# Optimization experiments

Measured on AMD Instinct MI355X. Metric: run time of the kernel, lower is better.

The kernel has to match this reference:

```python
import jax, jax.numpy as jnp
import numpy as np
from jax import lax

K = 100  # self.k in the module


def setup_inputs() -> dict:
    key = jax.random.key(0)
    k1, k2 = jax.random.split(key)
    query_batch = jax.random.normal(k1, (4, 64, 128), dtype=jnp.float32)  # [B,T,Z]
    targets = jax.random.normal(k2, (100000, 128), dtype=jnp.float32)     # [M,Z]
    return {"query_batch": query_batch, "targets": targets}


def _knn_emissions(query_batch, targets):
    # Brute-force L2 kNN (faiss.IndexFlatL2.search equivalent).
    # sqdist[b,t,m] = ||q_bt - target_m||^2
    qn = jnp.sum(query_batch * query_batch, -1)          # [B,T]
    tn = jnp.sum(targets * targets, -1)                  # [M]
    dots = jnp.einsum('btz,mz->btm', query_batch, targets)
    sqdist = qn[..., None] + tn[None, None, :] - 2.0 * dots  # [B,T,M]
    neg_d, idx = lax.top_k(-sqdist, K)                   # k smallest distances
    distances = -neg_d                                   # [B,T,K]
    # probabilities = exp(-d) / sum exp(-d)  == softmax(-d)
    emit_p = jax.nn.softmax(-distances, axis=-1)         # [B,T,K]
    states = targets[idx]                                # [B,T,K,Z]
    return emit_p, states


def _transition_probs(states):
    # Banded transitions: only between the K states of step t and step t+1.
    # transition_probability(a, b) = exp(-||a-b||^2)  (Gaussian L2 kernel)
    a = states[:, :-1]                                   # [B,T-1,K,Z]
    b = states[:, 1:]                                    # [B,T-1,K,Z]
    d = jnp.sum(a * a, -1)[..., :, None] + jnp.sum(b * b, -1)[..., None, :] \
        - 2.0 * jnp.einsum('btiz,btjz->btij', a, b)      # [B,T-1,K,K]
    return jnp.exp(-d)


def _viterbi_single(emit_p, trans_p):
    # emit_p [T,K], trans_p [T-1,K,K] -> best path indices [T] (int32)
    v0 = emit_p[0]

    def step(v, inp):
        tr, em = inp                                     # [K,K], [K]
        scores = v[:, None] * tr                         # [K,K]
        best = scores.max(axis=0)
        back = jnp.argmax(scores, axis=0)                # [K]
        v_new = best * em
        # rescale to avoid underflow over long T; argmax path unchanged
        v_new = v_new / jnp.maximum(v_new.max(), jnp.float32(1e-30))
        return v_new, back

    v_last, backptrs = lax.scan(step, v0, (trans_p, emit_p[1:]))
    last = jnp.argmax(v_last).astype(jnp.int32)

    def back_step(idx, bp):
        prev = bp[idx].astype(jnp.int32)
        return prev, prev

    _, path_head = lax.scan(back_step, last, backptrs, reverse=True)  # [T-1]
    return jnp.concatenate([path_head, last[None]])      # [T]


def reference(query_batch, targets):
    emit_p, states = _knn_emissions(query_batch, targets)
    trans_p = _transition_probs(states)
    paths = jax.vmap(_viterbi_single)(emit_p, trans_p)   # [B,T]
    # gather selected reference states: [B,T,Z]
    out = jnp.take_along_axis(states, paths[..., None, None], axis=2)[:, :, 0, :]
    return out
```

## Files before the change

kernel.cpp:

```cpp
#include <hip/hip_runtime.h>
#include <cfloat>
#include <climits>
#include <cstdint>
#include <cstddef>

#define ZD    128
#define NQ    256
#define NB    4
#define NT    64
#define KK    100
#define CAP   2048
#define NSAMP 4096
#define RANK  24
#define EPS   3.0f
#define SLABS 256
#define BKT   24
#define TROWS 64
#define QROWS 128
#define LPAD  136

typedef __attribute__((ext_vector_type(8))) short  short8;
typedef __attribute__((ext_vector_type(4))) float  floatx4;
typedef unsigned long long u64;

__device__ inline unsigned short f2bf(float f) {
  unsigned u = __builtin_bit_cast(unsigned, f);
  unsigned r = u + 0x7fffu + ((u >> 16) & 1u);
  return (unsigned short)(r >> 16);
}
__device__ inline unsigned fkey(float f) {
  unsigned u = __builtin_bit_cast(unsigned, f);
  unsigned m = (u & 0x80000000u) ? 0xFFFFFFFFu : 0x80000000u;
  return u ^ m;
}
__device__ inline float unfkey(unsigned k) {
  unsigned u = (k & 0x80000000u) ? (k ^ 0x80000000u) : ~k;
  return __builtin_bit_cast(float, u);
}

__global__ __launch_bounds__(256) void k0_norms(
    const float* __restrict__ Q, const float* __restrict__ T, int M,
    float* __restrict__ qn, float* __restrict__ tn) {
  int gid = blockIdx.x * 256 + threadIdx.x;
  if (gid < M) {
    const float* r = T + (size_t)gid * ZD;
    float s = 0.f;
    #pragma unroll
    for (int z4 = 0; z4 < 32; ++z4) {
      float4 v = *(const float4*)&r[z4 * 4];
      s = fmaf(v.x, v.x, s); s = fmaf(v.y, v.y, s);
      s = fmaf(v.z, v.z, s); s = fmaf(v.w, v.w, s);
    }
    tn[gid] = s;
  } else if (gid < M + NQ) {
    int q = gid - M;
    const float* r = Q + (size_t)q * ZD;
    float s = 0.f;
    #pragma unroll
    for (int z4 = 0; z4 < 32; ++z4) {
      float4 v = *(const float4*)&r[z4 * 4];
      s = fmaf(v.x, v.x, s); s = fmaf(v.y, v.y, s);
      s = fmaf(v.z, v.z, s); s = fmaf(v.w, v.w, s);
    }
    qn[q] = s;
  }
}

__global__ __launch_bounds__(256) void k1a_mfma(
    const float* __restrict__ Q, const float* __restrict__ T,
    const float* __restrict__ qn, const float* __restrict__ tn,
    float* __restrict__ sd_g) {
  __shared__ short Ts[TROWS * LPAD];
  __shared__ short Qs[QROWS * LPAD];
  const int tid = threadIdx.x;
  const int m0 = blockIdx.x * TROWS;
  const int qbase = blockIdx.y * QROWS;

  #pragma unroll
  for (int it = 0; it < 16; ++it) {
    int li = tid + it * 256;
    int row = li >> 5, z4 = li & 31;
    float4 v = *(const float4*)&Q[(size_t)(qbase + row) * ZD + z4 * 4];
    unsigned lo = (unsigned)f2bf(v.x) | ((unsigned)f2bf(v.y) << 16);
    unsigned hi = (unsigned)f2bf(v.z) | ((unsigned)f2bf(v.w) << 16);
    *(uint2*)&Qs[row * LPAD + z4 * 4] = make_uint2(lo, hi);
  }
  #pragma unroll
  for (int it = 0; it < 8; ++it) {
    int li = tid + it * 256;
    int row = li >> 5, z4 = li & 31;
    float4 v = *(const float4*)&T[(size_t)(m0 + row) * ZD + z4 * 4];
    unsigned lo = (unsigned)f2bf(v.x) | ((unsigned)f2bf(v.y) << 16);
    unsigned hi = (unsigned)f2bf(v.z) | ((unsigned)f2bf(v.w) << 16);
    *(uint2*)&Ts[row * LPAD + z4 * 4] = make_uint2(lo, hi);
  }
  __syncthreads();

  const int wave = tid >> 6;
  const int lane = tid & 63;
  const int quad = lane >> 4;
  const int n16  = lane & 15;

  floatx4 acc[8];
  #pragma unroll
  for (int qt = 0; qt < 8; ++qt) acc[qt] = (floatx4)0.f;
  #pragma unroll
  for (int ks = 0; ks < 4; ++ks) {
    short8 a = *(const short8*)&Ts[(wave * 16 + n16) * LPAD + ks * 32 + quad * 8];
    #pragma unroll
    for (int qt = 0; qt < 8; ++qt) {
      short8 b = *(const short8*)&Qs[(qt * 16 + n16) * LPAD + ks * 32 + quad * 8];
      acc[qt] = __builtin_amdgcn_mfma_f32_16x16x32_bf16(a, b, acc[qt], 0, 0, 0);
    }
  }

  const int mbase = m0 + wave * 16 + quad * 4;
  const float4 tnv = *(const float4*)&tn[mbase];
  #pragma unroll
  for (int qt = 0; qt < 8; ++qt) {
    const int q = qbase + qt * 16 + n16;
    const float base = qn[q];
    float4 dv;
    dv.x = fmaf(-2.0f, acc[qt][0], base + tnv.x);
    dv.y = fmaf(-2.0f, acc[qt][1], base + tnv.y);
    dv.z = fmaf(-2.0f, acc[qt][2], base + tnv.z);
    dv.w = fmaf(-2.0f, acc[qt][3], base + tnv.w);
    *(float4*)&sd_g[(size_t)q * NSAMP + mbase] = dv;
  }
}

__global__ __launch_bounds__(256) void k1b_pick(
    const float* __restrict__ sd_g, float* __restrict__ thr) {
  __shared__ float red[256];
  __shared__ int   hist[256];
  const int q = blockIdx.x, tid = threadIdx.x;
  const float* sd = sd_g + (size_t)q * NSAMP;
  float vals[16];
  float lm = FLT_MAX;
  #pragma unroll
  for (int k = 0; k < 16; ++k) {
    vals[k] = sd[k * 256 + tid];
    lm = fminf(lm, vals[k]);
  }
  red[tid] = lm;
  hist[tid] = 0;
  __syncthreads();
  for (int o = 128; o > 0; o >>= 1) {
    if (tid < o) red[tid] = fminf(red[tid], red[tid + o]);
    __syncthreads();
  }
  const float dmin = red[0];
  __syncthreads();
  #pragma unroll
  for (int k = 0; k < 16; ++k) {
    int b = (int)((vals[k] - dmin) * 3.2f);
    b = b < 0 ? 0 : (b > 255 ? 255 : b);
    atomicAdd(&hist[b], 1);
  }
  __syncthreads();
  if (tid == 0) {
    int cum = 0; float Tq = dmin + 80.0f;
    for (int b = 0; b < 256; ++b) {
      cum += hist[b];
      if (cum >= RANK) { Tq = dmin + (float)(b + 1) * 0.3125f; break; }
    }
    thr[q] = Tq;
  }
}

__global__ __launch_bounds__(256, 4) void k2_mfma(
    const float* __restrict__ Q, const float* __restrict__ T, int M, int slabn,
    const float* __restrict__ qn, const float* __restrict__ tn,
    const float* __restrict__ thr,
    int* __restrict__ cnt2, int* __restrict__ sure2, int* __restrict__ cand) {
  __shared__ short Ts[TROWS * LPAD];
  __shared__ short Qs[QROWS * LPAD];
  __shared__ int   lcnt[QROWS];
  __shared__ int   lsure[QROWS];
  __shared__ int   lent[QROWS * BKT];
  const int tid = threadIdx.x;
  const int slab = blockIdx.x;
  const int qbase = blockIdx.y * QROWS;
  const int sbeg = slab * slabn;
  const int send = min(sbeg + slabn, M);

  #pragma unroll
  for (int it = 0; it < 16; ++it) {
    int li = tid + it * 256;
    int row = li >> 5, z4 = li & 31;
    float4 v = *(const float4*)&Q[(size_t)(qbase + row) * ZD + z4 * 4];
    unsigned lo = (unsigned)f2bf(v.x) | ((unsigned)f2bf(v.y) << 16);
    unsigned hi = (unsigned)f2bf(v.z) | ((unsigned)f2bf(v.w) << 16);
    *(uint2*)&Qs[row * LPAD + z4 * 4] = make_uint2(lo, hi);
  }
  if (tid < QROWS) { lcnt[tid] = 0; lsure[tid] = 0; }

  const int wave = tid >> 6;
  const int lane = tid & 63;
  const int quad = lane >> 4;
  const int n16  = lane & 15;

  float baseq[8], tqp[8], tqm[8];
  #pragma unroll
  for (int qt = 0; qt < 8; ++qt) {
    const int q = qbase + qt * 16 + n16;
    float b = qn[q], Tq = thr[q];
    baseq[qt] = b; tqp[qt] = Tq + EPS; tqm[qt] = Tq - EPS;
  }

  float4 pf[8];
  #pragma unroll
  for (int it = 0; it < 8; ++it) {
    int li = tid + it * 256;
    int row = li >> 5, z4 = li & 31;
    int m = sbeg + row;
    pf[it] = make_float4(0.f, 0.f, 0.f, 0.f);
    if (m < send) pf[it] = *(const float4*)&T[(size_t)m * ZD + z4 * 4];
  }

  for (int m0 = sbeg; m0 < send; m0 += TROWS) {
    __syncthreads();
    #pragma unroll
    for (int it = 0; it < 8; ++it) {
      int li = tid + it * 256;
      int row = li >> 5, z4 = li & 31;
      unsigned lo = (unsigned)f2bf(pf[it].x) | ((unsigned)f2bf(pf[it].y) << 16);
      unsigned hi = (unsigned)f2bf(pf[it].z) | ((unsigned)f2bf(pf[it].w) << 16);
      *(uint2*)&Ts[row * LPAD + z4 * 4] = make_uint2(lo, hi);
    }
    __syncthreads();
    if (m0 + TROWS < send) {
      #pragma unroll
      for (int it = 0; it < 8; ++it) {
        int li = tid + it * 256;
        int row = li >> 5, z4 = li & 31;
        int m = m0 + TROWS + row;
        pf[it] = make_float4(0.f, 0.f, 0.f, 0.f);
        if (m < send) pf[it] = *(const float4*)&T[(size_t)m * ZD + z4 * 4];
      }
    }

    floatx4 acc[8];
    #pragma unroll
    for (int qt = 0; qt < 8; ++qt) acc[qt] = (floatx4)0.f;
    #pragma unroll
    for (int ks = 0; ks < 4; ++ks) {
      short8 a = *(const short8*)&Ts[(wave * 16 + n16) * LPAD + ks * 32 + quad * 8];
      #pragma unroll
      for (int qt = 0; qt < 8; ++qt) {
        short8 b = *(const short8*)&Qs[(qt * 16 + n16) * LPAD + ks * 32 + quad * 8];
        acc[qt] = __builtin_amdgcn_mfma_f32_16x16x32_bf16(a, b, acc[qt], 0, 0, 0);
      }
    }

    const int mbase = m0 + wave * 16 + quad * 4;
    float4 tnv = make_float4(0.f, 0.f, 0.f, 0.f);
    if (mbase + 3 < M) tnv = *(const float4*)&tn[mbase];
    else {
      if (mbase + 0 < M) tnv.x = tn[mbase + 0];
      if (mbase + 1 < M) tnv.y = tn[mbase + 1];
      if (mbase + 2 < M) tnv.z = tn[mbase + 2];
    }
    const float tns[4] = {tnv.x, tnv.y, tnv.z, tnv.w};
    #pragma unroll
    for (int qt = 0; qt < 8; ++qt) {
      const int ql = qt * 16 + n16;
      #pragma unroll
      for (int r = 0; r < 4; ++r) {
        const int m = mbase + r;
        float dap = fmaf(-2.0f, acc[qt][r], baseq[qt] + tns[r]);
        if (m < send && dap < tqp[qt]) {
          int pos = atomicAdd(&lcnt[ql], 1);
          if (pos < BKT) lent[ql * BKT + pos] = m;
          if (dap < tqm[qt]) atomicAdd(&lsure[ql], 1);
        }
      }
    }
  }
  __syncthreads();
  if (tid < QROWS) {
    cnt2 [(size_t)(qbase + tid) * SLABS + slab] = lcnt[tid];
    sure2[(size_t)(qbase + tid) * SLABS + slab] = lsure[tid];
  }
  for (int li = tid; li < QROWS * BKT; li += 256) {
    int ql = li / BKT, j = li % BKT;
    int c = lcnt[ql]; if (c > BKT) c = BKT;
    if (j < c)
      cand[((size_t)(qbase + ql) * SLABS + slab) * BKT + j] = lent[li];
  }
}

__global__ __launch_bounds__(256) void k3a_scan(
    const int* __restrict__ cnt2, const int* __restrict__ sure2,
    int* __restrict__ scanx, int* __restrict__ totals, int* __restrict__ validf) {
  const int q = blockIdx.x, tid = threadIdx.x;
  __shared__ int sscan[256];
  __shared__ int ssure, sovf;
  int c = cnt2[(size_t)q * SLABS + tid];
  int su = sure2[(size_t)q * SLABS + tid];
  if (tid == 0) { ssure = 0; sovf = 0; }
  __syncthreads();
  atomicAdd(&ssure, su);
  if (c > BKT) atomicOr(&sovf, 1);
  int val = c;
  sscan[tid] = val;
  __syncthreads();
  for (int o = 1; o < 256; o <<= 1) {
    int add = (tid >= o) ? sscan[tid - o] : 0;
    __syncthreads();
    val += add;
    sscan[tid] = val;
    __syncthreads();
  }
  scanx[(size_t)q * SLABS + tid] = val - c;
  const int total = sscan[255];
  if (tid == 0) {
    totals[q] = total;
    validf[q] = (sovf == 0 && ssure >= KK && total <= CAP) ? 1 : 0;
  }
}

__global__ __launch_bounds__(256) void k3b_rescore(
    const float* __restrict__ Q, const float* __restrict__ T,
    const float* __restrict__ qn, const float* __restrict__ tn,
    const int* __restrict__ cnt2, const int* __restrict__ cand,
    const int* __restrict__ scanx, const int* __restrict__ validf,
    u64* __restrict__ keys) {
  const int q = blockIdx.x, ch = blockIdx.y, tid = threadIdx.x;
  if (!validf[q]) return;
  __shared__ float qv[ZD];
  for (int z = tid; z < ZD; z += 256) qv[z] = Q[(size_t)q * ZD + z];
  __syncthreads();
  const float qnv = qn[q];
  const int slab = ch * 64 + (tid >> 2);
  const int lane = tid & 3;
  const int c = min(cnt2[(size_t)q * SLABS + slab], BKT);
  const int off = scanx[(size_t)q * SLABS + slab];
  for (int k = lane; k < c; k += 4) {
    int idx = cand[((size_t)q * SLABS + slab) * BKT + k];
    const float* r = T + (size_t)idx * ZD;
    float dot = 0.f;
    #pragma unroll 4
    for (int z4 = 0; z4 < 32; ++z4) {
      float4 v = *(const float4*)&r[z4 * 4];
      dot = fmaf(qv[z4 * 4 + 0], v.x, dot);
      dot = fmaf(qv[z4 * 4 + 1], v.y, dot);
      dot = fmaf(qv[z4 * 4 + 2], v.z, dot);
      dot = fmaf(qv[z4 * 4 + 3], v.w, dot);
    }
    float d = fmaf(-2.0f, dot, qnv + tn[idx]);
    keys[(size_t)q * CAP + off + k] = ((u64)fkey(d) << 32) | (unsigned)idx;
  }
}

__global__ __launch_bounds__(256) void k3c_select(
    const float* __restrict__ Q, const float* __restrict__ T, int M,
    const float* __restrict__ qn, const float* __restrict__ tn,
    const int* __restrict__ totals, const int* __restrict__ validf,
    const u64* __restrict__ keys_g,
    int* __restrict__ topi, float* __restrict__ emit) {
  __shared__ u64 key[CAP];
  __shared__ u64 buf[256];
  __shared__ unsigned redA[256], redB[256];
  __shared__ int hist[256];
  __shared__ int hscan[256];
  __shared__ float qv[ZD];
  __shared__ float cd[256];
  __shared__ float sdF[KK];
  __shared__ int   siF[KK];
  __shared__ float ebuf[KK];
  __shared__ float ssum;
  __shared__ int Bb, C2, ccnt, srcFlag;
  __shared__ unsigned kminS; __shared__ int shiftS;
  const int q = blockIdx.x, tid = threadIdx.x;
  const int total = totals[q];
  const bool valid = validf[q] != 0;

  if (valid) {
    for (int i = tid; i < CAP; i += 256)
      key[i] = (i < total) ? keys_g[(size_t)q * CAP + i] : ~0ULL;
    unsigned lmin = 0xFFFFFFFFu, lmax = 0u;
    for (int i = tid; i < total; i += 256) {
      unsigned h = (unsigned)(key[i] >> 32);
      lmin = min(lmin, h); lmax = max(lmax, h);
    }
    redA[tid] = lmin; redB[tid] = lmax;
    hist[tid] = 0;
    __syncthreads();
    for (int o = 128; o > 0; o >>= 1) {
      if (tid < o) {
        redA[tid] = min(redA[tid], redA[tid + o]);
        redB[tid] = max(redB[tid], redB[tid + o]);
      }
      __syncthreads();
    }
    if (tid == 0) {
      unsigned range = redB[0] - redA[0];
      int s = 0;
      while ((range >> s) > 255u) ++s;
      kminS = redA[0]; shiftS = s;
      ccnt = 0;
    }
    __syncthreads();
    const unsigned kmin = kminS; const int sh = shiftS;
    for (int i = tid; i < total; i += 256) {
      int b = (int)(((unsigned)(key[i] >> 32) - kmin) >> sh);
      atomicAdd(&hist[b], 1);
    }
    __syncthreads();
    int v0 = hist[tid];
    hscan[tid] = v0;
    __syncthreads();
    for (int o = 1; o < 256; o <<= 1) {
      int add = (tid >= o) ? hscan[tid - o] : 0;
      __syncthreads();
      v0 += add;
      hscan[tid] = v0;
      __syncthreads();
    }
    if (hscan[tid] >= KK && (tid == 0 || hscan[tid - 1] < KK)) {
      Bb = tid; C2 = hscan[tid];
    }
    __syncthreads();
    const int B = Bb, c2 = C2;
    if (c2 <= 256) {
      for (int i = tid; i < total; i += 256) {
        int b = (int)(((unsigned)(key[i] >> 32) - kmin) >> sh);
        if (b <= B) { int pos = atomicAdd(&ccnt, 1); buf[pos] = key[i]; }
      }
      __syncthreads();
      if (tid >= c2) buf[tid] = ~0ULL;
      __syncthreads();
      for (int k = 2; k <= 256; k <<= 1) {
        for (int j = k >> 1; j > 0; j >>= 1) {
          int x = tid ^ j;
          if (x > tid) {
            u64 a = buf[tid], b2 = buf[x];
            bool asc = ((tid & k) == 0);
            if ((a > b2) == asc) { buf[tid] = b2; buf[x] = a; }
          }
          __syncthreads();
        }
      }
      if (tid == 0) srcFlag = 0;
    } else {
      for (int k = 2; k <= CAP; k <<= 1) {
        for (int j = k >> 1; j > 0; j >>= 1) {
          for (int t = tid; t < CAP; t += 256) {
            int x = t ^ j;
            if (x > t) {
              u64 a = key[t], b2 = key[x];
              bool asc = ((t & k) == 0);
              if ((a > b2) == asc) { key[t] = b2; key[x] = a; }
            }
          }
          __syncthreads();
        }
      }
      if (tid == 0) srcFlag = 1;
    }
    __syncthreads();
  } else {
    for (int z = tid; z < ZD; z += 256) qv[z] = Q[(size_t)q * ZD + z];
    if (tid == 0) {
      for (int k = 0; k < KK; ++k) { sdF[k] = FLT_MAX; siF[k] = INT_MAX; }
      srcFlag = 0;
    }
    __syncthreads();
    const float qnv = qn[q];
    for (int base = 0; base < M; base += 256) {
      int m = base + tid; float d = FLT_MAX;
      if (m < M) {
        const float* r = T + (size_t)m * ZD;
        float dot = 0.f;
        for (int z = 0; z < ZD; ++z) dot = fmaf(qv[z], r[z], dot);
        d = fmaf(-2.0f, dot, qnv + tn[m]);
      }
      cd[tid] = d;
      __syncthreads();
      if (tid == 0) {
        for (int e = 0; e < 256; ++e) {
          float dd = cd[e]; int mm = base + e;
          if (dd < sdF[KK - 1] || (dd == sdF[KK - 1] && mm < siF[KK - 1])) {
            int pos = KK - 1;
            while (pos > 0 && (sdF[pos - 1] > dd || (sdF[pos - 1] == dd && siF[pos - 1] > mm))) {
              sdF[pos] = sdF[pos - 1]; siF[pos] = siF[pos - 1]; --pos;
            }
            sdF[pos] = dd; siF[pos] = mm;
          }
        }
      }
      __syncthreads();
    }
    if (tid < KK) buf[tid] = ((u64)fkey(sdF[tid]) << 32) | (unsigned)siF[tid];
    __syncthreads();
  }

  const int sf = srcFlag;
  if (tid == 0) {
    u64 k0v = sf ? key[0] : buf[0];
    float d0 = unfkey((unsigned)(k0v >> 32));
    float sum = 0.f;
    for (int k = 0; k < KK; ++k) {
      u64 kk = sf ? key[k] : buf[k];
      float e = expf(d0 - unfkey((unsigned)(kk >> 32)));
      ebuf[k] = e; sum += e;
    }
    ssum = sum;
  }
  __syncthreads();
  if (tid < KK) {
    u64 kk = sf ? key[tid] : buf[tid];
    emit[(size_t)q * KK + tid] = ebuf[tid] / ssum;
    topi[(size_t)q * KK + tid] = (int)(kk & 0xFFFFFFFFu);
  }
}

__global__ __launch_bounds__(256) void k4_trans(
    const float* __restrict__ T, const int* __restrict__ topi,
    float* __restrict__ trans) {
  const int bt = blockIdx.x;
  const int b = bt / (NT - 1), t = bt % (NT - 1);
  const int* iA = topi + (size_t)(b * NT + t) * KK;
  const int* iB = topi + (size_t)(b * NT + t + 1) * KK;
  __shared__ float As[KK * 132];
  __shared__ float Bs[KK * 132];
  __shared__ float an[KK];
  __shared__ float bn[KK];
  const int tid = threadIdx.x;
  for (int li = tid; li < KK * 32; li += 256) {
    int row = li >> 5, z4 = li & 31;
    *(float4*)&As[row * 132 + z4 * 4] = *(const float4*)&T[(size_t)iA[row] * ZD + z4 * 4];
    *(float4*)&Bs[row * 132 + z4 * 4] = *(const float4*)&T[(size_t)iB[row] * ZD + z4 * 4];
  }
  __syncthreads();
  if (tid < KK) {
    float s = 0.f;
    for (int z = 0; z < ZD; ++z) s = fmaf(As[tid * 132 + z], As[tid * 132 + z], s);
    an[tid] = s;
  } else if (tid < 2 * KK) {
    int r = tid - KK;
    float s = 0.f;
    for (int z = 0; z < ZD; ++z) s = fmaf(Bs[r * 132 + z], Bs[r * 132 + z], s);
    bn[r] = s;
  }
  __syncthreads();
  const int tx = tid & 15, ty = tid >> 4;
  float acc[7][7];
  #pragma unroll
  for (int k = 0; k < 7; ++k)
    #pragma unroll
    for (int m = 0; m < 7; ++m) acc[k][m] = 0.f;
  int rr[7], cc[7];
  #pragma unroll
  for (int k = 0; k < 7; ++k) { rr[k] = min(ty + 16 * k, KK - 1); cc[k] = min(tx + 16 * k, KK - 1); }
  for (int z4 = 0; z4 < 32; ++z4) {
    float4 a[7], bb[7];
    #pragma unroll
    for (int k = 0; k < 7; ++k) a[k] = *(const float4*)&As[rr[k] * 132 + z4 * 4];
    #pragma unroll
    for (int m = 0; m < 7; ++m) bb[m] = *(const float4*)&Bs[cc[m] * 132 + z4 * 4];
    #pragma unroll
    for (int k = 0; k < 7; ++k)
      #pragma unroll
      for (int m = 0; m < 7; ++m) {
        acc[k][m] = fmaf(a[k].x, bb[m].x, acc[k][m]);
        acc[k][m] = fmaf(a[k].y, bb[m].y, acc[k][m]);
        acc[k][m] = fmaf(a[k].z, bb[m].z, acc[k][m]);
        acc[k][m] = fmaf(a[k].w, bb[m].w, acc[k][m]);
      }
  }
  float* trow = trans + (size_t)bt * KK * KK;
  #pragma unroll
  for (int k = 0; k < 7; ++k) {
    int r = ty + 16 * k;
    if (r < KK) {
      #pragma unroll
      for (int m = 0; m < 7; ++m) {
        int c = tx + 16 * m;
        if (c < KK) {
          float d = fmaf(-2.0f, acc[k][m], an[r] + bn[c]);
          trow[r * KK + c] = expf(-d);
        }
      }
    }
  }
}

__global__ __launch_bounds__(256) void k5_viterbi(
    const float* __restrict__ T, const int* __restrict__ topi,
    const float* __restrict__ emit, const float* __restrict__ trans,
    float* __restrict__ out) {
  const int b = blockIdx.x, tid = threadIdx.x;
  __shared__ float trS[KK * KK];
  __shared__ float v[KK], vn[KK];
  __shared__ float pb[200];
  __shared__ int   pi[200];
  __shared__ int   bpS[(NT - 1) * KK];
  __shared__ int   path[NT];
  __shared__ float maxsh;
  __shared__ int   zflag;

  float4 r[10];
  {
    const float* tr0 = trans + (size_t)(b * (NT - 1)) * KK * KK;
    #pragma unroll
    for (int i = 0; i < 10; ++i) {
      int li = tid + i * 256;
      if (li < 2500) r[i] = *(const float4*)&tr0[li * 4];
    }
  }
  if (tid < KK) v[tid] = emit[(size_t)(b * NT) * KK + tid];
  if (tid == 0) zflag = 0;
  __syncthreads();

  for (int t = 1; t < NT; ++t) {
    #pragma unroll
    for (int i = 0; i < 10; ++i) {
      int li = tid + i * 256;
      if (li < 2500) *(float4*)&trS[li * 4] = r[i];
    }
    __syncthreads();
    if (t < NT - 1) {
      const float* trn = trans + (size_t)(b * (NT - 1) + t) * KK * KK;
      #pragma unroll
      for (int i = 0; i < 10; ++i) {
        int li = tid + i * 256;
        if (li < 2500) r[i] = *(const float4*)&trn[li * 4];
      }
    }
    if (tid < 200) {
      const int j = tid % 100, half = tid / 100;
      const int ia = half * 50, ibnd = ia + 50;
      float best = -FLT_MAX; int bi = ia;
      for (int i = ia; i < ibnd; ++i) {
        float s = v[i] * trS[i * KK + j];
        if (s > best) { best = s; bi = i; }
      }
      pb[tid] = best; pi[tid] = bi;
    }
    __syncthreads();
    if (tid < KK) {
      float b0 = pb[tid], b1 = pb[100 + tid];
      int   i0 = pi[tid], i1 = pi[100 + tid];
      float best = b0; int bi = i0;
      if (b1 > b0) { best = b1; bi = i1; }
      vn[tid] = best * emit[(size_t)(b * NT + t) * KK + tid];
      bpS[(t - 1) * KK + tid] = bi;
    }
    __syncthreads();
    if (tid == 0) {
      float m = vn[0];
      for (int j = 1; j < KK; ++j) m = fmaxf(m, vn[j]);
      maxsh = m;
      if (m == 0.0f) zflag = 1;
    }
    __syncthreads();
    if (tid < KK) v[tid] = vn[tid] / fmaxf(maxsh, 1e-30f);
    __syncthreads();
    if (zflag) {
      for (int li = tid; li < (NT - 1 - t) * KK; li += 256)
        bpS[t * KK + li] = 0;
      __syncthreads();
      break;
    }
  }
  if (tid == 0) {
    float best = -FLT_MAX; int last = 0;
    for (int j = 0; j < KK; ++j) if (v[j] > best) { best = v[j]; last = j; }
    path[NT - 1] = last;
    for (int tt = NT - 2; tt >= 0; --tt)
      path[tt] = bpS[tt * KK + path[tt + 1]];
  }
  __syncthreads();
  for (int li = tid; li < NT * ZD; li += 256) {
    int t = li >> 7, z = li & 127;
    out[(size_t)(b * NT + t) * ZD + z] =
        T[(size_t)topi[(size_t)(b * NT + t) * KK + path[t]] * ZD + z];
  }
}

extern "C" void kernel_launch(void* const* d_in, const int* in_sizes, int n_in,
                              void* d_out, int out_size, void* d_ws, size_t ws_size,
                              hipStream_t stream) {
  const float* Q = (const float*)d_in[0];
  const float* T = (const float*)d_in[1];
  float* out = (float*)d_out;
  const int M = in_sizes[1] / ZD;
  const int slabn = (M + SLABS - 1) / SLABS;

  char* p = (char*)d_ws;
  auto alloc = [&](size_t bytes) -> char* {
    char* r = p; p += (bytes + 511) & ~(size_t)511; return r;
  };
  float* qn     = (float*)alloc((size_t)NQ * 4);
  float* tn     = (float*)alloc((size_t)M * 4);
  float* thr    = (float*)alloc((size_t)NQ * 4);
  float* sd_g   = (float*)alloc((size_t)NQ * NSAMP * 4);
  int*   cnt2   = (int*)  alloc((size_t)NQ * SLABS * 4);
  int*   sure2  = (int*)  alloc((size_t)NQ * SLABS * 4);
  int*   cand   = (int*)  alloc((size_t)NQ * SLABS * BKT * 4);
  int*   scanx  = (int*)  alloc((size_t)NQ * SLABS * 4);
  int*   totals = (int*)  alloc((size_t)NQ * 4);
  int*   validf = (int*)  alloc((size_t)NQ * 4);
  u64*   keys   = (u64*)  alloc((size_t)NQ * CAP * 8);
  int*   topi   = (int*)  alloc((size_t)NQ * KK * 4);
  float* emit   = (float*)alloc((size_t)NQ * KK * 4);
  float* trans  = (float*)alloc((size_t)NB * (NT - 1) * KK * KK * 4);

  const int g0 = (M + NQ + 255) / 256;
  k0_norms<<<g0, 256, 0, stream>>>(Q, T, M, qn, tn);
  dim3 g1a(NSAMP / TROWS, NQ / QROWS);
  k1a_mfma<<<g1a, 256, 0, stream>>>(Q, T, qn, tn, sd_g);
  k1b_pick<<<NQ, 256, 0, stream>>>(sd_g, thr);
  dim3 g2(SLABS, NQ / QROWS);
  k2_mfma<<<g2, 256, 0, stream>>>(Q, T, M, slabn, qn, tn, thr, cnt2, sure2, cand);
  k3a_scan<<<NQ, 256, 0, stream>>>(cnt2, sure2, scanx, totals, validf);
  dim3 g3b(NQ, 4);
  k3b_rescore<<<g3b, 256, 0, stream>>>(Q, T, qn, tn, cnt2, cand, scanx, validf, keys);
  k3c_select<<<NQ, 256, 0, stream>>>(Q, T, M, qn, tn, totals, validf, keys, topi, emit);
  k4_trans<<<NB * (NT - 1), 256, 0, stream>>>(T, topi, trans);
  k5_viterbi<<<NB, 256, 0, stream>>>(T, topi, emit, trans, out);
}
```

Measured before the change: 250.8 us.

## Halve query tile in k2 and drop register prefetch of target rows

The k2 filtering kernel now processes 64 queries per block instead of 128, doubling the grid to 1024 blocks and halving per-block accumulators, LDS, and atomics. The software register prefetch of the next target tile is removed, so target loads now happen directly before the LDS store in each iteration. This is meant to improve parallelism and cut register pressure. In exchange, each target tile is read from memory twice as often and there is no longer any overlap of global loads with MFMA work.

```diff
diff --git a/kernel.cpp b/kernel.cpp
--- a/kernel.cpp
+++ b/kernel.cpp
@@ -17,6 +17,7 @@
 #define BKT   24
 #define TROWS 64
 #define QROWS 128
+#define QR2   64
 #define LPAD  136
 
 typedef __attribute__((ext_vector_type(8))) short  short8;
@@ -168,24 +169,24 @@
   }
 }
 
-__global__ __launch_bounds__(256, 4) void k2_mfma(
+__global__ __launch_bounds__(256, 3) void k2_mfma(
     const float* __restrict__ Q, const float* __restrict__ T, int M, int slabn,
     const float* __restrict__ qn, const float* __restrict__ tn,
     const float* __restrict__ thr,
     int* __restrict__ cnt2, int* __restrict__ sure2, int* __restrict__ cand) {
   __shared__ short Ts[TROWS * LPAD];
-  __shared__ short Qs[QROWS * LPAD];
-  __shared__ int   lcnt[QROWS];
-  __shared__ int   lsure[QROWS];
-  __shared__ int   lent[QROWS * BKT];
+  __shared__ short Qs[QR2 * LPAD];
+  __shared__ int   lcnt[QR2];
+  __shared__ int   lsure[QR2];
+  __shared__ int   lent[QR2 * BKT];
   const int tid = threadIdx.x;
   const int slab = blockIdx.x;
-  const int qbase = blockIdx.y * QROWS;
+  const int qbase = blockIdx.y * QR2;
   const int sbeg = slab * slabn;
   const int send = min(sbeg + slabn, M);
 
   #pragma unroll
-  for (int it = 0; it < 16; ++it) {
+  for (int it = 0; it < 8; ++it) {
     int li = tid + it * 256;
     int row = li >> 5, z4 = li & 31;
     float4 v = *(const float4*)&Q[(size_t)(qbase + row) * ZD + z4 * 4];
@@ -193,61 +194,44 @@
     unsigned hi = (unsigned)f2bf(v.z) | ((unsigned)f2bf(v.w) << 16);
     *(uint2*)&Qs[row * LPAD + z4 * 4] = make_uint2(lo, hi);
   }
-  if (tid < QROWS) { lcnt[tid] = 0; lsure[tid] = 0; }
+  if (tid < QR2) { lcnt[tid] = 0; lsure[tid] = 0; }
 
   const int wave = tid >> 6;
   const int lane = tid & 63;
   const int quad = lane >> 4;
   const int n16  = lane & 15;
 
-  float baseq[8], tqp[8], tqm[8];
-  #pragma unroll
-  for (int qt = 0; qt < 8; ++qt) {
+  float baseq[4], tqp[4], tqm[4];
+  #pragma unroll
+  for (int qt = 0; qt < 4; ++qt) {
     const int q = qbase + qt * 16 + n16;
     float b = qn[q], Tq = thr[q];
     baseq[qt] = b; tqp[qt] = Tq + EPS; tqm[qt] = Tq - EPS;
   }
 
-  float4 pf[8];
-  #pragma unroll
-  for (int it = 0; it < 8; ++it) {
-    int li = tid + it * 256;
-    int row = li >> 5, z4 = li & 31;
-    int m = sbeg + row;
-    pf[it] = make_float4(0.f, 0.f, 0.f, 0.f);
-    if (m < send) pf[it] = *(const float4*)&T[(size_t)m * ZD + z4 * 4];
-  }
-
   for (int m0 = sbeg; m0 < send; m0 += TROWS) {
     __syncthreads();
     #pragma unroll
     for (int it = 0; it < 8; ++it) {
       int li = tid + it * 256;
       int row = li >> 5, z4 = li & 31;
-      unsigned lo = (unsigned)f2bf(pf[it].x) | ((unsigned)f2bf(pf[it].y) << 16);
-      unsigned hi = (unsigned)f2bf(pf[it].z) | ((unsigned)f2bf(pf[it].w) << 16);
+      int m = m0 + row;
+      float4 v = make_float4(0.f, 0.f, 0.f, 0.f);
+      if (m < send) v = *(const float4*)&T[(size_t)m * ZD + z4 * 4];
+      unsigned lo = (unsigned)f2bf(v.x) | ((unsigned)f2bf(v.y) << 16);
+      unsigned hi = (unsigned)f2bf(v.z) | ((unsigned)f2bf(v.w) << 16);
       *(uint2*)&Ts[row * LPAD + z4 * 4] = make_uint2(lo, hi);
     }
     __syncthreads();
-    if (m0 + TROWS < send) {
-      #pragma unroll
-      for (int it = 0; it < 8; ++it) {
-        int li = tid + it * 256;
-        int row = li >> 5, z4 = li & 31;
-        int m = m0 + TROWS + row;
-        pf[it] = make_float4(0.f, 0.f, 0.f, 0.f);
-        if (m < send) pf[it] = *(const float4*)&T[(size_t)m * ZD + z4 * 4];
-      }
-    }
-
-    floatx4 acc[8];
-    #pragma unroll
-    for (int qt = 0; qt < 8; ++qt) acc[qt] = (floatx4)0.f;
+
+    floatx4 acc[4];
+    #pragma unroll
+    for (int qt = 0; qt < 4; ++qt) acc[qt] = (floatx4)0.f;
     #pragma unroll
     for (int ks = 0; ks < 4; ++ks) {
       short8 a = *(const short8*)&Ts[(wave * 16 + n16) * LPAD + ks * 32 + quad * 8];
       #pragma unroll
-      for (int qt = 0; qt < 8; ++qt) {
+      for (int qt = 0; qt < 4; ++qt) {
         short8 b = *(const short8*)&Qs[(qt * 16 + n16) * LPAD + ks * 32 + quad * 8];
         acc[qt] = __builtin_amdgcn_mfma_f32_16x16x32_bf16(a, b, acc[qt], 0, 0, 0);
       }
@@ -263,7 +247,7 @@
     }
     const float tns[4] = {tnv.x, tnv.y, tnv.z, tnv.w};
     #pragma unroll
-    for (int qt = 0; qt < 8; ++qt) {
+    for (int qt = 0; qt < 4; ++qt) {
       const int ql = qt * 16 + n16;
       #pragma unroll
       for (int r = 0; r < 4; ++r) {
@@ -278,11 +262,11 @@
     }
   }
   __syncthreads();
-  if (tid < QROWS) {
+  if (tid < QR2) {
     cnt2 [(size_t)(qbase + tid) * SLABS + slab] = lcnt[tid];
     sure2[(size_t)(qbase + tid) * SLABS + slab] = lsure[tid];
   }
-  for (int li = tid; li < QROWS * BKT; li += 256) {
+  for (int li = tid; li < QR2 * BKT; li += 256) {
     int ql = li / BKT, j = li % BKT;
     int c = lcnt[ql]; if (c > BKT) c = BKT;
     if (j < c)
@@ -713,7 +697,7 @@
   dim3 g1a(NSAMP / TROWS, NQ / QROWS);
   k1a_mfma<<<g1a, 256, 0, stream>>>(Q, T, qn, tn, sd_g);
   k1b_pick<<<NQ, 256, 0, stream>>>(sd_g, thr);
-  dim3 g2(SLABS, NQ / QROWS);
+  dim3 g2(SLABS, NQ / QR2);
   k2_mfma<<<g2, 256, 0, stream>>>(Q, T, M, slabn, qn, tn, thr, cnt2, sure2, cand);
   k3a_scan<<<NQ, 256, 0, stream>>>(cnt2, sure2, scanx, totals, validf);
   dim3 g3b(NQ, 4);
```

After: 282.7 us. 12.7% more time.
